# Optimization experiments

Measured on AMD Instinct MI355X. Metric: run time of the kernel, lower is better.

The kernel has to match this reference:

```python
import jax, jax.numpy as jnp
import numpy as np

BN_EPS = 1e-5
Q_EPS = 1e-8

def quant_weight(w):
    # per-output-channel median-abs scale, ternary quantization
    s = jnp.median(jnp.abs(w).reshape(w.shape[0], -1), axis=1)
    s = jnp.maximum(s, Q_EPS)[:, None, None, None]
    return jnp.clip(jnp.round(w / s), -1.0, 1.0) * s

def bitconv(x, w, b, stride, pad):
    wq = quant_weight(w)
    y = jax.lax.conv_general_dilated(
        x, wq, (stride, stride), [(pad, pad), (pad, pad)],
        dimension_numbers=('NCHW', 'OIHW', 'NCHW'))
    return y + b[None, :, None, None]

def bn(x, g, b, m, v):
    scale = g / jnp.sqrt(v + BN_EPS)
    return x * scale[None, :, None, None] + (b - m * scale)[None, :, None, None]

def setup_inputs() -> dict:
    key = jax.random.key(0)
    ks = jax.random.split(key, 20)
    B, Cin, H, W = 64, 1024, 14, 14
    width, Cout = 256, 1024  # planes=256, expansion=4
    d = {}
    d['x'] = jax.random.normal(ks[0], (B, Cin, H, W), jnp.float32)
    d['w1'] = jax.random.normal(ks[1], (width, Cin, 1, 1), jnp.float32) * 0.05
    d['b1'] = jax.random.normal(ks[2], (width,), jnp.float32) * 0.01
    d['g1'] = jax.random.uniform(ks[3], (width,), jnp.float32, 0.5, 1.5)
    d['be1'] = jax.random.normal(ks[4], (width,), jnp.float32) * 0.1
    d['m1'] = jax.random.normal(ks[5], (width,), jnp.float32) * 0.1
    d['v1'] = jax.random.uniform(ks[6], (width,), jnp.float32, 0.5, 1.5)
    d['w2'] = jax.random.normal(ks[7], (width, width, 3, 3), jnp.float32) * 0.05
    d['b2'] = jax.random.normal(ks[8], (width,), jnp.float32) * 0.01
    d['g2'] = jax.random.uniform(ks[9], (width,), jnp.float32, 0.5, 1.5)
    d['be2'] = jax.random.normal(ks[10], (width,), jnp.float32) * 0.1
    d['m2'] = jax.random.normal(ks[11], (width,), jnp.float32) * 0.1
    d['v2'] = jax.random.uniform(ks[12], (width,), jnp.float32, 0.5, 1.5)
    d['w3'] = jax.random.normal(ks[13], (Cout, width, 1, 1), jnp.float32) * 0.05
    d['b3'] = jax.random.normal(ks[14], (Cout,), jnp.float32) * 0.01
    d['g3'] = jax.random.uniform(ks[15], (Cout,), jnp.float32, 0.5, 1.5)
    d['be3'] = jax.random.normal(ks[16], (Cout,), jnp.float32) * 0.1
    d['m3'] = jax.random.normal(ks[17], (Cout,), jnp.float32) * 0.1
    d['v3'] = jax.random.uniform(ks[18], (Cout,), jnp.float32, 0.5, 1.5)
    return d

def reference(x, w1, b1, g1, be1, m1, v1,
              w2, b2, g2, be2, m2, v2,
              w3, b3, g3, be3, m3, v3):
    out = jax.nn.silu(bn(bitconv(x, w1, b1, 1, 0), g1, be1, m1, v1))
    out = jax.nn.silu(bn(bitconv(out, w2, b2, 1, 1), g2, be2, m2, v2))
    out = bn(bitconv(out, w3, b3, 1, 0), g3, be3, m3, v3)
    return jax.nn.silu(out + x)
```

## Files before the change

kernel.cpp:

```cpp
#include <hip/hip_runtime.h>
#include <cstdint>
#include <cstddef>

typedef unsigned short u16;
typedef unsigned int u32;
typedef __attribute__((ext_vector_type(4))) float f32x4;
typedef __attribute__((ext_vector_type(8))) short s16x8;

__device__ __forceinline__ u16 f2bf(float f) {
  u32 u = __float_as_uint(f);
  u = (u + 0x7fffu + ((u >> 16) & 1u)) >> 16;
  return (u16)u;
}

__device__ __forceinline__ float silu_f(float y) {
  return y / (1.0f + __expf(-y));
}

template<int N, int REMAP>
__global__ __launch_bounds__(256) void quant_kernel(
    const float* __restrict__ w, const float* __restrict__ bias,
    const float* __restrict__ g, const float* __restrict__ be,
    const float* __restrict__ mu, const float* __restrict__ var,
    u16* __restrict__ wq, float* __restrict__ alpha, float* __restrict__ beta)
{
  constexpr int NV = N / 64;
  __shared__ int hist[4 * 256];

  const int tid = threadIdx.x;
  const int wave = tid >> 6;
  const int lane = tid & 63;
  const int ch = blockIdx.x * 4 + wave;
  const int wb = wave * 256;

  u32 vals[NV];
  const float* wp = w + (size_t)ch * N;
  #pragma unroll
  for (int t = 0; t < NV; ++t)
    vals[t] = __float_as_uint(wp[lane + 64 * t]);

  const int r0 = N / 2;
  int r = r0;
  u32 prefix = 0;
  #pragma unroll
  for (int pass = 0; pass < 4; ++pass) {
    const int shift = 24 - 8 * pass;
    hist[wb + lane] = 0;
    hist[wb + 64 + lane] = 0;
    hist[wb + 128 + lane] = 0;
    hist[wb + 192 + lane] = 0;
    __syncthreads();
    #pragma unroll
    for (int t = 0; t < NV; ++t) {
      u32 a = vals[t] & 0x7fffffffu;
      bool cand;
      if (pass == 0) cand = true;
      else cand = ((a >> (shift + 8)) == (prefix >> (shift + 8)));
      if (cand) atomicAdd(&hist[wb + ((a >> shift) & 255)], 1);
    }
    __syncthreads();
    int h0 = hist[wb + 4 * lane + 0];
    int h1 = hist[wb + 4 * lane + 1];
    int h2 = hist[wb + 4 * lane + 2];
    int h3 = hist[wb + 4 * lane + 3];
    int s4 = h0 + h1 + h2 + h3;
    int cum = s4;
    #pragma unroll
    for (int off = 1; off < 64; off <<= 1) {
      int tt = __shfl_up(cum, off);
      if (lane >= off) cum += tt;
    }
    int pre = cum - s4;
    bool sel = (r > pre) && (r <= cum);
    unsigned long long bal = __ballot(sel);
    int src = __ffsll((unsigned long long)bal) - 1;
    int c0 = pre + h0, c1 = c0 + h1, c2 = c1 + h2;
    int d_l, nr_l;
    if (r <= c0)      { d_l = 4 * lane + 0; nr_l = r - pre; }
    else if (r <= c1) { d_l = 4 * lane + 1; nr_l = r - c0; }
    else if (r <= c2) { d_l = 4 * lane + 2; nr_l = r - c1; }
    else              { d_l = 4 * lane + 3; nr_l = r - c2; }
    int d = __shfl(d_l, src);
    r = __shfl(nr_l, src);
    prefix |= (u32)d << shift;
    __syncthreads();
  }
  const u32 v0 = prefix;

  int cle = 0;
  u32 mn = 0xFFFFFFFFu;
  #pragma unroll
  for (int t = 0; t < NV; ++t) {
    u32 a = vals[t] & 0x7fffffffu;
    cle += (a <= v0) ? 1 : 0;
    if (a > v0) mn = min(mn, a);
  }
  #pragma unroll
  for (int off = 1; off < 64; off <<= 1) {
    cle += __shfl_xor(cle, off);
    mn = min(mn, (u32)__shfl_xor((int)mn, off));
  }
  u32 v1 = (cle >= r0 + 1) ? v0 : mn;

  float s = 0.5f * (__uint_as_float(v0) + __uint_as_float(v1));
  s = fmaxf(s, 1e-8f);

  #pragma unroll
  for (int t = 0; t < NV; ++t) {
    int i = lane + 64 * t;
    float q = rintf(__uint_as_float(vals[t]) / s);
    q = fminf(fmaxf(q, -1.0f), 1.0f);
    int oi;
    if (REMAP) {
      int cin = i / 9, tap = i - cin * 9;
      oi = tap * 256 + cin;
    } else {
      oi = i;
    }
    wq[(size_t)ch * N + oi] = f2bf(q);
  }
  if (lane == 0) {
    float sc = g[ch] / sqrtf(var[ch] + 1e-5f);
    alpha[ch] = s * sc;
    beta[ch] = (bias[ch] - mu[ch]) * sc + be[ch];
  }
}

__global__ __launch_bounds__(256) void transpose_cast_kernel(
    const float* __restrict__ x, u16* __restrict__ xb)
{
  __shared__ u16 tile[64 * 198];
  const int n = blockIdx.x;
  const int c0 = blockIdx.y * 64;
  const float* xp = x + ((size_t)n * 1024 + c0) * 196;
  for (int i = threadIdx.x; i < 64 * 196; i += 256) {
    int c = i / 196, hw = i - c * 196;
    tile[c * 198 + hw] = f2bf(xp[i]);
  }
  __syncthreads();
  u16* op = xb + (size_t)n * 196 * 1024 + c0;
  for (int i = threadIdx.x; i < 64 * 196; i += 256) {
    int hw = i >> 6, c = i & 63;
    op[(size_t)hw * 1024 + c] = tile[c * 198 + hw];
  }
}

template<int MODE, int KTOT, int BJ>
__global__ __launch_bounds__(256, 2) void gemm_kernel(
    const u16* __restrict__ Wq, const u16* __restrict__ Bact,
    const float* __restrict__ alpha, const float* __restrict__ beta,
    u16* __restrict__ outb, float* __restrict__ outf, const float* __restrict__ xres)
{
  constexpr int BK = 64;
  constexpr int NKT = KTOT / BK;
  constexpr int NI = BJ / 32;
  constexpr int SMEM_SIZE = (MODE == 3) ? 34816 : (16384 + BJ * BK * 2 + BJ * 4 + 1024);

  __shared__ __align__(16) char smem[SMEM_SIZE];
  u16* As = (u16*)smem;
  u16* Bs = (u16*)(smem + 16384);
  int* rowbase = (int*)(smem + 16384 + BJ * BK * 2);
  float* aS = (float*)(MODE == 3 ? (smem + 33792) : (smem + 16384 + BJ * BK * 2 + BJ * 4));
  float* bS = aS + 128;
  float* lbuf = (float*)smem;

  const int tid = threadIdx.x;
  const int jb = blockIdx.x * BJ;
  const int cb = blockIdx.y * 128;
  const int wave = tid >> 6;
  const int lane = tid & 63;
  const int wm = (wave & 1) * 64;
  const int wn = (wave >> 1) * (BJ / 2);
  const int quad = lane >> 4;
  const int l16 = lane & 15;

  if (tid < 128) {
    aS[tid] = alpha[cb + tid];
    bS[tid] = beta[cb + tid];
  }
  if (MODE == 2 && tid < BJ) {
    int j = jb + tid;
    int n = j / 196, hw = j - n * 196;
    int h = hw / 14, w = hw - h * 14;
    rowbase[tid] = ((n * 16 + h) * 16 + w) * 256;
  }
  __syncthreads();

  f32x4 acc[4][NI];
  #pragma unroll
  for (int a = 0; a < 4; ++a)
    #pragma unroll
    for (int b = 0; b < NI; ++b)
      acc[a][b] = {0.f, 0.f, 0.f, 0.f};

  const int row_s = tid >> 3;
  const int cc_s = tid & 7;

  for (int kt = 0; kt < NKT; ++kt) {
    {
      const uint4* gp = reinterpret_cast<const uint4*>(Wq + (size_t)cb * KTOT + kt * BK);
      #pragma unroll
      for (int i = 0; i < 4; ++i) {
        int row = row_s + 32 * i;
        uint4 v = gp[(size_t)row * (KTOT / 8) + cc_s];
        *reinterpret_cast<uint4*>(&As[row * BK + ((cc_s ^ (row & 7)) << 3)]) = v;
      }
    }
    if (MODE == 2) {
      int tap = kt >> 2;
      int c0 = (kt & 3) * 64;
      int dy = tap / 3, dx = tap - dy * 3;
      int tapoff = (dy * 16 + dx) * 256 + c0;
      const uint4* gp = reinterpret_cast<const uint4*>(Bact);
      #pragma unroll
      for (int i = 0; i < BJ / 32; ++i) {
        int row = row_s + 32 * i;
        uint4 v = gp[((rowbase[row] + tapoff) >> 3) + cc_s];
        *reinterpret_cast<uint4*>(&Bs[row * BK + ((cc_s ^ (row & 7)) << 3)]) = v;
      }
    } else {
      const uint4* gp = reinterpret_cast<const uint4*>(Bact + (size_t)jb * KTOT + kt * BK);
      #pragma unroll
      for (int i = 0; i < BJ / 32; ++i) {
        int row = row_s + 32 * i;
        uint4 v = gp[(size_t)row * (KTOT / 8) + cc_s];
        *reinterpret_cast<uint4*>(&Bs[row * BK + ((cc_s ^ (row & 7)) << 3)]) = v;
      }
    }
    __syncthreads();

    #pragma unroll
    for (int s = 0; s < 2; ++s) {
      s16x8 af[4], bf[NI];
      #pragma unroll
      for (int mi = 0; mi < 4; ++mi) {
        int row = wm + mi * 16 + l16;
        int kc = s * 4 + quad;
        af[mi] = *reinterpret_cast<const s16x8*>(&As[row * BK + ((kc ^ (row & 7)) << 3)]);
      }
      #pragma unroll
      for (int ni = 0; ni < NI; ++ni) {
        int row = wn + ni * 16 + l16;
        int kc = s * 4 + quad;
        bf[ni] = *reinterpret_cast<const s16x8*>(&Bs[row * BK + ((kc ^ (row & 7)) << 3)]);
      }
      #pragma unroll
      for (int mi = 0; mi < 4; ++mi)
        #pragma unroll
        for (int ni = 0; ni < NI; ++ni)
          acc[mi][ni] = __builtin_amdgcn_mfma_f32_16x16x32_bf16(af[mi], bf[ni], acc[mi][ni], 0, 0, 0);
    }
    __syncthreads();
  }

  if (MODE == 1 || MODE == 2) {
    #pragma unroll
    for (int mi = 0; mi < 4; ++mi) {
      const int lc = wm + mi * 16 + quad * 4;
      #pragma unroll
      for (int ni = 0; ni < NI; ++ni) {
        const int j = jb + wn + ni * 16 + l16;
        ushort4 pk;
        float y;
        y = silu_f(aS[lc + 0] * acc[mi][ni][0] + bS[lc + 0]); pk.x = f2bf(y);
        y = silu_f(aS[lc + 1] * acc[mi][ni][1] + bS[lc + 1]); pk.y = f2bf(y);
        y = silu_f(aS[lc + 2] * acc[mi][ni][2] + bS[lc + 2]); pk.z = f2bf(y);
        y = silu_f(aS[lc + 3] * acc[mi][ni][3] + bS[lc + 3]); pk.w = f2bf(y);
        size_t base;
        if (MODE == 1) {
          int n = j / 196, hw = j - n * 196;
          int h = hw / 14, w = hw - h * 14;
          base = (size_t)(((n * 16 + h + 1) * 16) + (w + 1)) * 256 + cb + lc;
        } else {
          base = (size_t)j * 256 + cb + lc;
        }
        *reinterpret_cast<ushort4*>(&outb[base]) = pk;
      }
    }
  } else {
    #pragma unroll
    for (int k = 0; k < 2; ++k) {
      if ((wave & 1) == k) {
        #pragma unroll
        for (int mi = 0; mi < 4; ++mi) {
          const int cl = mi * 16 + quad * 4;
          const int gc = 64 * k + cl;
          #pragma unroll
          for (int ni = 0; ni < 4; ++ni) {
            const int jj = wn + ni * 16 + l16;
            #pragma unroll
            for (int r = 0; r < 4; ++r)
              lbuf[(cl + r) * 132 + jj] = aS[gc + r] * acc[mi][ni][r] + bS[gc + r];
          }
        }
      }
      __syncthreads();
      #pragma unroll
      for (int it = 0; it < 8; ++it) {
        int idx = tid + it * 256;
        int cl = idx >> 5;
        int jg = idx & 31;
        int c = cb + 64 * k + cl;
        int j0 = jb + jg * 4;
        int n = j0 / 196, hw = j0 - n * 196;
        size_t o = (size_t)n * 200704 + (size_t)c * 196 + hw;
        float4 lv = *reinterpret_cast<float4*>(&lbuf[cl * 132 + jg * 4]);
        float4 xv = *reinterpret_cast<const float4*>(&xres[o]);
        float4 ov;
        ov.x = silu_f(lv.x + xv.x);
        ov.y = silu_f(lv.y + xv.y);
        ov.z = silu_f(lv.z + xv.z);
        ov.w = silu_f(lv.w + xv.w);
        *reinterpret_cast<float4*>(&outf[o]) = ov;
      }
      __syncthreads();
    }
  }
}

extern "C" void kernel_launch(void* const* d_in, const int* in_sizes, int n_in,
                              void* d_out, int out_size, void* d_ws, size_t ws_size,
                              hipStream_t stream)
{
  const float* x   = (const float*)d_in[0];
  const float* w1  = (const float*)d_in[1];
  const float* b1  = (const float*)d_in[2];
  const float* g1  = (const float*)d_in[3];
  const float* be1 = (const float*)d_in[4];
  const float* m1  = (const float*)d_in[5];
  const float* v1  = (const float*)d_in[6];
  const float* w2  = (const float*)d_in[7];
  const float* b2  = (const float*)d_in[8];
  const float* g2  = (const float*)d_in[9];
  const float* be2 = (const float*)d_in[10];
  const float* m2  = (const float*)d_in[11];
  const float* v2  = (const float*)d_in[12];
  const float* w3  = (const float*)d_in[13];
  const float* b3  = (const float*)d_in[14];
  const float* g3  = (const float*)d_in[15];
  const float* be3 = (const float*)d_in[16];
  const float* m3  = (const float*)d_in[17];
  const float* v3  = (const float*)d_in[18];
  float* out = (float*)d_out;

  uint8_t* ws = (uint8_t*)d_ws;
  u16* xb    = (u16*)(ws);
  u16* act1p = (u16*)(ws + 25690112ull);
  u16* act2  = (u16*)(ws + 34078720ull);
  u16* w1q   = (u16*)(ws + 40501248ull);
  u16* w2q   = (u16*)(ws + 41025536ull);
  u16* w3q   = (u16*)(ws + 42205184ull);
  float* a1c = (float*)(ws + 42729472ull);
  float* b1c = a1c + 256;
  float* a2c = b1c + 256;
  float* b2c = a2c + 256;
  float* a3c = b2c + 256;
  float* b3c = a3c + 1024;

  hipMemsetAsync(act1p, 0, 8388608ull, stream);

  transpose_cast_kernel<<<dim3(64, 16), 256, 0, stream>>>(x, xb);
  quant_kernel<1024, 0><<<64, 256, 0, stream>>>(w1, b1, g1, be1, m1, v1, w1q, a1c, b1c);
  quant_kernel<2304, 1><<<64, 256, 0, stream>>>(w2, b2, g2, be2, m2, v2, w2q, a2c, b2c);
  quant_kernel<256, 0><<<256, 256, 0, stream>>>(w3, b3, g3, be3, m3, v3, w3q, a3c, b3c);

  gemm_kernel<1, 1024, 64><<<dim3(196, 2), 256, 0, stream>>>(w1q, xb, a1c, b1c, act1p, (float*)nullptr, (const float*)nullptr);
  gemm_kernel<2, 2304, 64><<<dim3(196, 2), 256, 0, stream>>>(w2q, act1p, a2c, b2c, act2, (float*)nullptr, (const float*)nullptr);
  gemm_kernel<3, 256, 128><<<dim3(98, 8), 256, 0, stream>>>(w3q, act2, a3c, b3c, (u16*)nullptr, out, x);
}
```

Baseline: 282.1 us.

## Use direct global-to-LDS loads in GEMM, vectorize transpose, one-wave quant blocks

The GEMM tile loads now use the global_load_lds builtin, so A and B tiles are written straight into LDS with an XOR swizzle folded into the precomputed per-lane global pointers. The per-block rowbase table and its extra barrier are dropped. The transpose-cast kernel reads float4 and writes packed 32-bit pairs instead of scalar accesses, and the quantization kernel runs one wave per block over more blocks. This targets register staging and load-instruction overhead, but direct LDS loads change ordering and wait semantics, and the swizzle mapping must still match the fragment reads.

```diff
diff --git a/kernel.cpp b/kernel.cpp
--- a/kernel.cpp
+++ b/kernel.cpp
@@ -17,21 +17,24 @@
   return y / (1.0f + __expf(-y));
 }
 
+__device__ __forceinline__ void gl_lds16(const u16* g, u16* l) {
+  __builtin_amdgcn_global_load_lds(
+      (const __attribute__((address_space(1))) void*)g,
+      (__attribute__((address_space(3))) void*)l, 16, 0, 0);
+}
+
 template<int N, int REMAP>
-__global__ __launch_bounds__(256) void quant_kernel(
+__global__ __launch_bounds__(64) void quant_kernel(
     const float* __restrict__ w, const float* __restrict__ bias,
     const float* __restrict__ g, const float* __restrict__ be,
     const float* __restrict__ mu, const float* __restrict__ var,
     u16* __restrict__ wq, float* __restrict__ alpha, float* __restrict__ beta)
 {
   constexpr int NV = N / 64;
-  __shared__ int hist[4 * 256];
-
-  const int tid = threadIdx.x;
-  const int wave = tid >> 6;
-  const int lane = tid & 63;
-  const int ch = blockIdx.x * 4 + wave;
-  const int wb = wave * 256;
+  __shared__ int hist[256];
+
+  const int lane = threadIdx.x;
+  const int ch = blockIdx.x;
 
   u32 vals[NV];
   const float* wp = w + (size_t)ch * N;
@@ -45,10 +48,10 @@
   #pragma unroll
   for (int pass = 0; pass < 4; ++pass) {
     const int shift = 24 - 8 * pass;
-    hist[wb + lane] = 0;
-    hist[wb + 64 + lane] = 0;
-    hist[wb + 128 + lane] = 0;
-    hist[wb + 192 + lane] = 0;
+    hist[lane] = 0;
+    hist[64 + lane] = 0;
+    hist[128 + lane] = 0;
+    hist[192 + lane] = 0;
     __syncthreads();
     #pragma unroll
     for (int t = 0; t < NV; ++t) {
@@ -56,13 +59,13 @@
       bool cand;
       if (pass == 0) cand = true;
       else cand = ((a >> (shift + 8)) == (prefix >> (shift + 8)));
-      if (cand) atomicAdd(&hist[wb + ((a >> shift) & 255)], 1);
-    }
-    __syncthreads();
-    int h0 = hist[wb + 4 * lane + 0];
-    int h1 = hist[wb + 4 * lane + 1];
-    int h2 = hist[wb + 4 * lane + 2];
-    int h3 = hist[wb + 4 * lane + 3];
+      if (cand) atomicAdd(&hist[(a >> shift) & 255], 1);
+    }
+    __syncthreads();
+    int h0 = hist[4 * lane + 0];
+    int h1 = hist[4 * lane + 1];
+    int h2 = hist[4 * lane + 2];
+    int h3 = hist[4 * lane + 3];
     int s4 = h0 + h1 + h2 + h3;
     int cum = s4;
     #pragma unroll
@@ -133,15 +136,20 @@
   const int n = blockIdx.x;
   const int c0 = blockIdx.y * 64;
   const float* xp = x + ((size_t)n * 1024 + c0) * 196;
-  for (int i = threadIdx.x; i < 64 * 196; i += 256) {
-    int c = i / 196, hw = i - c * 196;
-    tile[c * 198 + hw] = f2bf(xp[i]);
+  const float4* xp4 = reinterpret_cast<const float4*>(xp);
+  for (int i = threadIdx.x; i < 64 * 49; i += 256) {
+    int c = i / 49, hg = i - c * 49;
+    float4 v = xp4[i];
+    u16* t = &tile[c * 198 + hg * 4];
+    t[0] = f2bf(v.x); t[1] = f2bf(v.y); t[2] = f2bf(v.z); t[3] = f2bf(v.w);
   }
   __syncthreads();
-  u16* op = xb + (size_t)n * 196 * 1024 + c0;
-  for (int i = threadIdx.x; i < 64 * 196; i += 256) {
-    int hw = i >> 6, c = i & 63;
-    op[(size_t)hw * 1024 + c] = tile[c * 198 + hw];
+  u32* op = reinterpret_cast<u32*>(xb + (size_t)n * 196 * 1024 + c0);
+  for (int i = threadIdx.x; i < 196 * 32; i += 256) {
+    int hw = i >> 5, cp = i & 31;
+    u32 lo = tile[(cp * 2) * 198 + hw];
+    u32 hi = tile[(cp * 2 + 1) * 198 + hw];
+    op[hw * 512 + cp] = lo | (hi << 16);
   }
 }
 
@@ -154,13 +162,14 @@
   constexpr int BK = 64;
   constexpr int NKT = KTOT / BK;
   constexpr int NI = BJ / 32;
-  constexpr int SMEM_SIZE = (MODE == 3) ? 34816 : (16384 + BJ * BK * 2 + BJ * 4 + 1024);
+  constexpr int ACH = 4;
+  constexpr int BCH = BJ / 32;
+  constexpr int SMEM_SIZE = (MODE == 3) ? 34816 : 25600;
 
   __shared__ __align__(16) char smem[SMEM_SIZE];
   u16* As = (u16*)smem;
   u16* Bs = (u16*)(smem + 16384);
-  int* rowbase = (int*)(smem + 16384 + BJ * BK * 2);
-  float* aS = (float*)(MODE == 3 ? (smem + 33792) : (smem + 16384 + BJ * BK * 2 + BJ * 4));
+  float* aS = (float*)(MODE == 3 ? (smem + 33792) : (smem + 16384 + BJ * 128));
   float* bS = aS + 128;
   float* lbuf = (float*)smem;
 
@@ -173,18 +182,33 @@
   const int wn = (wave >> 1) * (BJ / 2);
   const int quad = lane >> 4;
   const int l16 = lane & 15;
+  const int lr = lane >> 3;
+  const int perm = (lane & 7) ^ lr;
+
+  const u16* gA[ACH];
+  #pragma unroll
+  for (int it = 0; it < ACH; ++it) {
+    int row = wave * 32 + it * 8 + lr;
+    gA[it] = Wq + (size_t)(cb + row) * KTOT + perm * 8;
+  }
+  const u16* gB[BCH];
+  #pragma unroll
+  for (int it = 0; it < BCH; ++it) {
+    int row = wave * (8 * BCH) + it * 8 + lr;
+    if (MODE == 2) {
+      int j = jb + row;
+      int n = j / 196, hw = j - n * 196;
+      int h = hw / 14, w = hw - h * 14;
+      gB[it] = Bact + (size_t)(((n * 16 + h) * 16 + w) * 256) + perm * 8;
+    } else {
+      gB[it] = Bact + (size_t)(jb + row) * KTOT + perm * 8;
+    }
+  }
 
   if (tid < 128) {
     aS[tid] = alpha[cb + tid];
     bS[tid] = beta[cb + tid];
   }
-  if (MODE == 2 && tid < BJ) {
-    int j = jb + tid;
-    int n = j / 196, hw = j - n * 196;
-    int h = hw / 14, w = hw - h * 14;
-    rowbase[tid] = ((n * 16 + h) * 16 + w) * 256;
-  }
-  __syncthreads();
 
   f32x4 acc[4][NI];
   #pragma unroll
@@ -193,39 +217,22 @@
     for (int b = 0; b < NI; ++b)
       acc[a][b] = {0.f, 0.f, 0.f, 0.f};
 
-  const int row_s = tid >> 3;
-  const int cc_s = tid & 7;
-
   for (int kt = 0; kt < NKT; ++kt) {
-    {
-      const uint4* gp = reinterpret_cast<const uint4*>(Wq + (size_t)cb * KTOT + kt * BK);
-      #pragma unroll
-      for (int i = 0; i < 4; ++i) {
-        int row = row_s + 32 * i;
-        uint4 v = gp[(size_t)row * (KTOT / 8) + cc_s];
-        *reinterpret_cast<uint4*>(&As[row * BK + ((cc_s ^ (row & 7)) << 3)]) = v;
-      }
-    }
+    #pragma unroll
+    for (int it = 0; it < ACH; ++it)
+      gl_lds16(gA[it] + kt * BK, As + (wave * ACH + it) * 512);
     if (MODE == 2) {
       int tap = kt >> 2;
       int c0 = (kt & 3) * 64;
       int dy = tap / 3, dx = tap - dy * 3;
       int tapoff = (dy * 16 + dx) * 256 + c0;
-      const uint4* gp = reinterpret_cast<const uint4*>(Bact);
-      #pragma unroll
-      for (int i = 0; i < BJ / 32; ++i) {
-        int row = row_s + 32 * i;
-        uint4 v = gp[((rowbase[row] + tapoff) >> 3) + cc_s];
-        *reinterpret_cast<uint4*>(&Bs[row * BK + ((cc_s ^ (row & 7)) << 3)]) = v;
-      }
+      #pragma unroll
+      for (int it = 0; it < BCH; ++it)
+        gl_lds16(gB[it] + tapoff, Bs + (wave * BCH + it) * 512);
     } else {
-      const uint4* gp = reinterpret_cast<const uint4*>(Bact + (size_t)jb * KTOT + kt * BK);
-      #pragma unroll
-      for (int i = 0; i < BJ / 32; ++i) {
-        int row = row_s + 32 * i;
-        uint4 v = gp[(size_t)row * (KTOT / 8) + cc_s];
-        *reinterpret_cast<uint4*>(&Bs[row * BK + ((cc_s ^ (row & 7)) << 3)]) = v;
-      }
+      #pragma unroll
+      for (int it = 0; it < BCH; ++it)
+        gl_lds16(gB[it] + kt * BK, Bs + (wave * BCH + it) * 512);
     }
     __syncthreads();
 
@@ -360,9 +367,9 @@
   hipMemsetAsync(act1p, 0, 8388608ull, stream);
 
   transpose_cast_kernel<<<dim3(64, 16), 256, 0, stream>>>(x, xb);
-  quant_kernel<1024, 0><<<64, 256, 0, stream>>>(w1, b1, g1, be1, m1, v1, w1q, a1c, b1c);
-  quant_kernel<2304, 1><<<64, 256, 0, stream>>>(w2, b2, g2, be2, m2, v2, w2q, a2c, b2c);
-  quant_kernel<256, 0><<<256, 256, 0, stream>>>(w3, b3, g3, be3, m3, v3, w3q, a3c, b3c);
+  quant_kernel<1024, 0><<<256, 64, 0, stream>>>(w1, b1, g1, be1, m1, v1, w1q, a1c, b1c);
+  quant_kernel<2304, 1><<<256, 64, 0, stream>>>(w2, b2, g2, be2, m2, v2, w2q, a2c, b2c);
+  quant_kernel<256, 0><<<1024, 64, 0, stream>>>(w3, b3, g3, be3, m3, v3, w3q, a3c, b3c);
 
   gemm_kernel<1, 1024, 64><<<dim3(196, 2), 256, 0, stream>>>(w1q, xb, a1c, b1c, act1p, (float*)nullptr, (const float*)nullptr);
   gemm_kernel<2, 2304, 64><<<dim3(196, 2), 256, 0, stream>>>(w2q, act1p, a2c, b2c, act2, (float*)nullptr, (const float*)nullptr);
```

Result: faster. 239.5 us (-15.1%).
